# Performance work log

Measured on AMD Instinct MI355X. Metric: run time of the kernel, lower is better.

## Reference

```python
import jax, jax.numpy as jnp
import numpy as np

DEPTH = 6


def _interp_linear(x, out_len):
    # x: [B, C, Lin] -> [B, C, out_len], PyTorch mode='linear', align_corners=False
    lin = x.shape[-1]
    scale = lin / out_len
    coords = (jnp.arange(out_len, dtype=x.dtype) + 0.5) * scale - 0.5
    coords = jnp.clip(coords, 0.0, lin - 1)
    lo = jnp.floor(coords).astype(jnp.int32)
    hi = jnp.minimum(lo + 1, lin - 1)
    w = (coords - lo.astype(x.dtype))
    return x[..., lo] * (1.0 - w) + x[..., hi] * w


def _scale_features(x, conv_w, conv_b):
    # x: [B, C, L]; conv_w: [DEPTH, C, C, 3]; conv_b: [DEPTH, C]
    B, C, L = x.shape
    out = x
    for idx in range(DEPTH):
        k = 2 ** (idx + 1)
        pooled = out.reshape(B, C, L // k, k).mean(-1)  # avg_pool1d(kernel=k, stride=k)
        conv = jax.lax.conv_general_dilated(
            pooled, conv_w[idx], window_strides=(1,), padding=((1, 1),),
            dimension_numbers=("NCH", "OIH", "NCH"))
        conv = jax.nn.relu(conv + conv_b[idx][None, :, None])
        out = out + _interp_linear(conv, L)
    return out


def setup_inputs() -> dict:
    key = jax.random.key(0)
    ks = jax.random.split(key, 8)
    N, C = 8192, 512
    s = 1.0 / np.sqrt(C)
    return {
        "features": jax.random.normal(ks[0], (N, C), jnp.float32),
        "Wq": jax.random.normal(ks[1], (C, C), jnp.float32) * s,
        "Wk": jax.random.normal(ks[2], (C, C), jnp.float32) * s,
        "Wv": jax.random.normal(ks[3], (C, C), jnp.float32) * s,
        "Wo": jax.random.normal(ks[4], (C, C), jnp.float32) * s,
        "conv_w": jax.random.normal(ks[5], (DEPTH, C, C, 3), jnp.float32) * (1.0 / np.sqrt(3 * C)),
        "conv_b": jnp.zeros((DEPTH, C), jnp.float32),
        "num_subgraphs": 32,
        "subgraph_len": 256,
    }


def reference(features, Wq, Wk, Wv, Wo, conv_w, conv_b, num_subgraphs, subgraph_len):
    B, L = num_subgraphs, subgraph_len
    N, C = features.shape
    H = 8
    D = C // H
    x = features.reshape(B, L, C)

    # --- per-subgraph multi-head attention (pre_norm path, bn = identity) ---
    q = (x @ Wq).reshape(B, L, H, D)
    k = (x @ Wk).reshape(B, L, H, D)
    v = (x @ Wv).reshape(B, L, H, D)
    scores = jnp.einsum("blhd,bmhd->bhlm", q, k) / jnp.sqrt(jnp.array(D, x.dtype))
    attn = jax.nn.softmax(scores, axis=-1)
    ctx = jnp.einsum("bhlm,bmhd->blhd", attn, v).reshape(B, L, C)
    out = x + ctx @ Wo  # residual (dropout = identity at eval)

    # --- batched ScaleFeatures over subgraphs (ts.scatter.batched equivalent) ---
    local = _scale_features(out.transpose(0, 2, 1), conv_w, conv_b).transpose(0, 2, 1)
    out = out + local
    return out.reshape(N, C)
```

## Files before the change

### kernel.cpp

```cpp
#include <hip/hip_runtime.h>
#include <hip/hip_bf16.h>

typedef __bf16 bf16;
typedef __attribute__((ext_vector_type(8))) __bf16 bf16x8;
typedef __attribute__((ext_vector_type(4))) float f32x4;

#define GLDS16(gp, lp) __builtin_amdgcn_global_load_lds( \
    (const __attribute__((address_space(1))) void*)(gp),  \
    (__attribute__((address_space(3))) void*)(lp), 16, 0, 0)

template<int EPI, int BN>
__global__ __launch_bounds__(512)
void gemm_bt(const bf16* __restrict__ A, int lda, long sAb, long sAh,
             const bf16* __restrict__ Bt, int ldb, long sBb, long sBh,
             void* __restrict__ Cp, int ldc, long sCb, long sCh, long zC,
             int KC, int tilesN, float scale)
{
    constexpr int CT = BN / 64;
    constexpr int CW = 16 * CT;

    __shared__ __align__(16) bf16 Al[2][128 * 32];
    __shared__ __align__(16) bf16 Bl[2][BN * 32];
    __shared__ float red[1024];

    const int t    = threadIdx.x;
    const int lane = t & 63;
    const int w    = t >> 6;
    const int wr   = w >> 2, wc = w & 3;
    const int tm = blockIdx.x / tilesN, tn = blockIdx.x % tilesN;
    const int row0 = tm * 128, col0 = tn * BN;
    const int bb = blockIdx.y >> 3, bh = blockIdx.y & 7;
    const int koff = blockIdx.z * KC;

    const bf16* Ab = A  + (long)bb * sAb + (long)bh * sAh;
    const bf16* Bb = Bt + (long)bb * sBb + (long)bh * sBh;

    const int sr = t >> 2;
    const int sc = (t & 3) * 8;
    const long aoff  = (long)(row0 + sr) * lda + koff + sc;
    const long boff0 = (long)(col0 + sr) * ldb + koff + sc;
    const long boff1 = (long)(col0 + 128 + sr) * ldb + koff + sc;

    f32x4 acc[4][CT];
#pragma unroll
    for (int i = 0; i < 4; i++)
#pragma unroll
        for (int j = 0; j < CT; j++) acc[i][j] = (f32x4){0.f, 0.f, 0.f, 0.f};

    const int fr = lane & 15, hi = lane >> 4;
    const int nt = KC >> 5;
    int cur = 0;

    auto STAGE = [&](int buf, int kk) {
        GLDS16(Ab + aoff + kk, &Al[buf][w * 512]);
        if constexpr (BN >= 128) {
            GLDS16(Bb + boff0 + kk, &Bl[buf][w * 512]);
            if constexpr (BN == 256)
                GLDS16(Bb + boff1 + kk, &Bl[buf][4096 + w * 512]);
        } else {
            if (w < 4) GLDS16(Bb + boff0 + kk, &Bl[buf][w * 512]);
        }
    };

    STAGE(0, 0);
    __syncthreads();

    for (int tt = 0; tt < nt; ++tt) {
        if (tt + 1 < nt) STAGE(cur ^ 1, (tt + 1) * 32);
        bf16x8 af[4], bfr[CT];
#pragma unroll
        for (int rt = 0; rt < 4; rt++)
            af[rt] = *(const bf16x8*)&Al[cur][(wr * 64 + rt * 16 + fr) * 32 + hi * 8];
#pragma unroll
        for (int ct = 0; ct < CT; ct++)
            bfr[ct] = *(const bf16x8*)&Bl[cur][(wc * CW + ct * 16 + fr) * 32 + hi * 8];
#pragma unroll
        for (int rt = 0; rt < 4; rt++)
#pragma unroll
            for (int ct = 0; ct < CT; ct++)
                acc[rt][ct] = __builtin_amdgcn_mfma_f32_16x16x32_bf16(
                    af[rt], bfr[ct], acc[rt][ct], 0, 0, 0);
        __syncthreads();
        cur ^= 1;
    }

    const long cbase = (long)bb * sCb + (long)bh * sCh + (long)blockIdx.z * zC;

    if constexpr (EPI == 4) {
#pragma unroll
        for (int rt = 0; rt < 4; rt++)
#pragma unroll
            for (int ct = 0; ct < CT; ct++) acc[rt][ct] *= scale;

        float m[4][4];
#pragma unroll
        for (int rt = 0; rt < 4; rt++)
#pragma unroll
            for (int j = 0; j < 4; j++) {
                float mm = acc[rt][0][j];
#pragma unroll
                for (int ct = 1; ct < CT; ct++) mm = fmaxf(mm, acc[rt][ct][j]);
#pragma unroll
                for (int off = 1; off < 16; off <<= 1)
                    mm = fmaxf(mm, __shfl_xor(mm, off));
                m[rt][j] = mm;
            }
        if (fr == 0) {
#pragma unroll
            for (int rt = 0; rt < 4; rt++)
#pragma unroll
                for (int j = 0; j < 4; j++)
                    red[wc * 128 + wr * 64 + rt * 16 + hi * 4 + j] = m[rt][j];
        }
        __syncthreads();
#pragma unroll
        for (int rt = 0; rt < 4; rt++)
#pragma unroll
            for (int j = 0; j < 4; j++) {
                const int rl = wr * 64 + rt * 16 + hi * 4 + j;
                m[rt][j] = fmaxf(fmaxf(red[rl], red[128 + rl]),
                                 fmaxf(red[256 + rl], red[384 + rl]));
            }
        float ss[4][4];
#pragma unroll
        for (int rt = 0; rt < 4; rt++)
#pragma unroll
            for (int j = 0; j < 4; j++) ss[rt][j] = 0.f;
#pragma unroll
        for (int rt = 0; rt < 4; rt++)
#pragma unroll
            for (int ct = 0; ct < CT; ct++)
#pragma unroll
                for (int j = 0; j < 4; j++) {
                    const float e = __expf(acc[rt][ct][j] - m[rt][j]);
                    acc[rt][ct][j] = e;
                    ss[rt][j] += e;
                }
#pragma unroll
        for (int rt = 0; rt < 4; rt++)
#pragma unroll
            for (int j = 0; j < 4; j++) {
#pragma unroll
                for (int off = 1; off < 16; off <<= 1)
                    ss[rt][j] += __shfl_xor(ss[rt][j], off);
            }
        if (fr == 0) {
#pragma unroll
            for (int rt = 0; rt < 4; rt++)
#pragma unroll
                for (int j = 0; j < 4; j++)
                    red[512 + wc * 128 + wr * 64 + rt * 16 + hi * 4 + j] = ss[rt][j];
        }
        __syncthreads();
#pragma unroll
        for (int rt = 0; rt < 4; rt++)
#pragma unroll
            for (int j = 0; j < 4; j++) {
                const int rl = wr * 64 + rt * 16 + hi * 4 + j;
                m[rt][j] = 1.f / (red[512 + rl] + red[640 + rl] +
                                  red[768 + rl] + red[896 + rl]);
            }
        bf16* P = (bf16*)Cp;
#pragma unroll
        for (int rt = 0; rt < 4; rt++)
#pragma unroll
            for (int j = 0; j < 4; j++) {
                const int row = row0 + wr * 64 + rt * 16 + hi * 4 + j;
#pragma unroll
                for (int ct = 0; ct < CT; ct++) {
                    const int col = col0 + wc * CW + ct * 16 + fr;
                    P[cbase + (long)row * ldc + col] = (bf16)(acc[rt][ct][j] * m[rt][j]);
                }
            }
        return;
    }

#pragma unroll
    for (int rt = 0; rt < 4; rt++) {
#pragma unroll
        for (int j = 0; j < 4; j++) {
            const int row = row0 + wr * 64 + rt * 16 + hi * 4 + j;
#pragma unroll
            for (int ct = 0; ct < CT; ct++) {
                const int col = col0 + wc * CW + ct * 16 + fr;
                const float v = acc[rt][ct][j];
                const long idx = cbase + (long)row * ldc + col;
                if constexpr (EPI == 0) {
                    ((bf16*)Cp)[idx] = (bf16)v;
                } else {
                    ((float*)Cp)[idx] = v * scale;
                }
            }
        }
    }
}

__global__ void reduce_partials(const float* __restrict__ part,
                                float* __restrict__ outb,
                                long stride4, int P, int n4)
{
    const int i = blockIdx.x * 256 + threadIdx.x;
    if (i >= n4) return;
    float4 s = ((const float4*)part)[i];
    for (int p = 1; p < P; p++) {
        const float4 v = ((const float4*)part)[(long)p * stride4 + i];
        s.x += v.x; s.y += v.y; s.z += v.z; s.w += v.w;
    }
    ((float4*)outb)[i] = s;
}

__global__ void cvt_f32_bf16(const float* __restrict__ in, bf16* __restrict__ out, int n4)
{
    const int i = blockIdx.x * 256 + threadIdx.x;
    if (i < n4) {
        const float4 v = *(const float4*)&in[(long)i * 4];
        union { bf16 h[4]; ushort4 u; } o;
        o.h[0] = (bf16)v.x; o.h[1] = (bf16)v.y; o.h[2] = (bf16)v.z; o.h[3] = (bf16)v.w;
        *(ushort4*)&out[(long)i * 4] = o.u;
    }
}

__global__ __launch_bounds__(256)
void wtrans(const float* __restrict__ Wq, const float* __restrict__ Wk,
            const float* __restrict__ Wv, const float* __restrict__ Wo,
            bf16* __restrict__ wqkv_t, bf16* __restrict__ wo_t)
{
    __shared__ __align__(16) float T[64][68];
    const int z = blockIdx.z;
    const float* src = (z == 0) ? Wq : (z == 1) ? Wk : (z == 2) ? Wv : Wo;
    bf16* dst = (z < 3) ? (wqkv_t + (long)z * 262144) : wo_t;
    const int r0 = blockIdx.x * 64, c0 = blockIdx.y * 64;
    const int t  = threadIdx.x;
    const int rl = t >> 2;
    const int cq = (t & 3) * 16;
#pragma unroll
    for (int i = 0; i < 4; i++) {
        const float4 v = *(const float4*)&src[(long)(r0 + rl) * 512 + c0 + cq + i * 4];
        T[cq + i * 4 + 0][rl] = v.x;
        T[cq + i * 4 + 1][rl] = v.y;
        T[cq + i * 4 + 2][rl] = v.z;
        T[cq + i * 4 + 3][rl] = v.w;
    }
    __syncthreads();
#pragma unroll
    for (int i = 0; i < 4; i++) {
        const float4 v = *(const float4*)&T[rl][cq + i * 4];
        union { bf16 h[4]; ushort4 u; } o;
        o.h[0] = (bf16)v.x; o.h[1] = (bf16)v.y; o.h[2] = (bf16)v.z; o.h[3] = (bf16)v.w;
        *(ushort4*)&dst[(long)(c0 + rl) * 512 + r0 + cq + i * 4] = o.u;
    }
}

__global__ __launch_bounds__(256)
void vtrans(const bf16* __restrict__ qkv, bf16* __restrict__ vt)
{
    __shared__ __align__(16) bf16 T[64][72];
    const int t  = threadIdx.x;
    const int l0 = blockIdx.x * 64, j0 = blockIdx.y * 64, b = blockIdx.z;
    const int r  = t >> 3;
    const int c8 = (t & 7) * 8;
#pragma unroll
    for (int p = 0; p < 2; p++) {
        const int rr = r + p * 32;
        bf16 v[8];
        *(uint4*)v = *(const uint4*)&qkv[(long)(b * 256 + l0 + rr) * 1536 + 1024 + j0 + c8];
#pragma unroll
        for (int i = 0; i < 8; i++) T[c8 + i][rr] = v[i];
    }
    __syncthreads();
#pragma unroll
    for (int p = 0; p < 2; p++) {
        const int rr = r + p * 32;
        const uint4 val = *(const uint4*)&T[rr][c8];
        *(uint4*)&vt[(long)(b * 512 + j0 + rr) * 256 + l0 + c8] = val;
    }
}

__device__ inline void ic_scatter(bf16* __restrict__ icb, int lp, int Ld, float pooled)
{
    const bf16 pb = (bf16)pooled;
    icb[(long)lp * 1536 + 1] = pb;
    if (lp + 1 < Ld) icb[(long)(lp + 1) * 1536] = pb;
    if (lp > 0)      icb[(long)(lp - 1) * 1536 + 2] = pb;
    if (lp == 0)      icb[0] = (bf16)0.f;
    if (lp == Ld - 1) icb[(long)(Ld - 1) * 1536 + 2] = (bf16)0.f;
}

__global__ void cascade_first(const float* __restrict__ features,
                              const float* __restrict__ p0,
                              const float* __restrict__ p1,
                              float* __restrict__ out,
                              float* __restrict__ sf,
                              bf16* __restrict__ ic)
{
    const int idx = blockIdx.x * 256 + threadIdx.x;
    const int c  = idx & 511;
    const int lp = (idx >> 9) & 127;
    const int b  = idx >> 16;
    const long e0 = (long)(b * 256 + lp * 2) * 512 + c;
    const long e1 = e0 + 512;
    const float a0 = features[e0] + p0[e0] + p1[e0];
    const float a1 = features[e1] + p0[e1] + p1[e1];
    out[e0] = a0; out[e1] = a1;
    sf[e0]  = a0; sf[e1]  = a1;
    ic_scatter(ic + (long)b * 128 * 1536 + (long)c * 3, lp, 128, (a0 + a1) * 0.5f);
}

__global__ void cascade_mid(const float* __restrict__ conv,
                            const float* __restrict__ bias_p,
                            float* __restrict__ sf,
                            bf16* __restrict__ ic,
                            int ldshift, int k, float invk, float scale)
{
    const int idx = blockIdx.x * 256 + threadIdx.x;
    const int Ld = 1 << ldshift;
    const int c  = idx & 511;
    const int lp = (idx >> 9) & (Ld - 1);
    const int b  = idx >> (9 + ldshift);
    const int Lprev = Ld << 1;
    const float bias = bias_p[c];
    float* sfp = sf + ((long)b * 256 + (long)lp * k) * 512 + c;
    const float* cvb = conv + (long)b * Lprev * 512 + c;
    float s = 0.f;
    for (int i = 0; i < k; i++) {
        const int j = lp * k + i;
        float coords = (j + 0.5f) * scale - 0.5f;
        coords = fminf(fmaxf(coords, 0.f), (float)(Lprev - 1));
        const int lo = (int)coords;
        const int hi2 = min(lo + 1, Lprev - 1);
        const float w = coords - (float)lo;
        const float vlo = fmaxf(cvb[(long)lo * 512] + bias, 0.f);
        const float vhi = fmaxf(cvb[(long)hi2 * 512] + bias, 0.f);
        const float v = sfp[(long)i * 512] + vlo * (1.f - w) + vhi * w;
        sfp[(long)i * 512] = v;
        s += v;
    }
    ic_scatter(ic + (long)b * Ld * 1536 + (long)c * 3, lp, Ld, s * invk);
}

__global__ void upsample_final(const float* __restrict__ conv,
                               const float* __restrict__ bias_p,
                               const float* __restrict__ sf,
                               float* __restrict__ outp)
{
    const int idx = blockIdx.x * 256 + threadIdx.x;
    const int c = idx & 511;
    const int j = (idx >> 9) & 255;
    const int b = idx >> 17;
    const float bias = bias_p[c];
    float coords = (j + 0.5f) * (4.f / 256.f) - 0.5f;
    coords = fminf(fmaxf(coords, 0.f), 3.f);
    const int lo = (int)coords;
    const int hi2 = min(lo + 1, 3);
    const float w = coords - (float)lo;
    const long rb = (long)b * 4 * 512 + c;
    const float vlo = fmaxf(conv[rb + (long)lo * 512] + bias, 0.f);
    const float vhi = fmaxf(conv[rb + (long)hi2 * 512] + bias, 0.f);
    outp[idx] = outp[idx] + sf[idx] + vlo * (1.f - w) + vhi * w;
}

static const long OFF_XB    = 0;
static const long OFF_WQKV  = 8388608;
static const long OFF_WO    = 9961472;
static const long OFF_WCONV = 10485760;
static const long OFF_QKV   = 19922944;
static const long OFF_VT    = 45088768;
static const long OFF_P     = 53477376;
static const long OFF_CTX   = 87031808;
static const long OFF_WPART = 95420416;
static const long OFF_IC    = 128974848;
static const long OFF_CONVA = 141557760;
static const long OFF_CONVB = 149946368;
static const long OFF_SF    = 154140672;

extern "C" void kernel_launch(void* const* d_in, const int* in_sizes, int n_in,
                              void* d_out, int out_size, void* d_ws, size_t ws_size,
                              hipStream_t stream)
{
    const float* features = (const float*)d_in[0];
    const float* Wq = (const float*)d_in[1];
    const float* Wk = (const float*)d_in[2];
    const float* Wv = (const float*)d_in[3];
    const float* Wo = (const float*)d_in[4];
    const float* conv_w = (const float*)d_in[5];
    const float* conv_b = (const float*)d_in[6];
    float* out = (float*)d_out;

    char* ws = (char*)d_ws;
    bf16* xb     = (bf16*)(ws + OFF_XB);
    bf16* wqkv_t = (bf16*)(ws + OFF_WQKV);
    bf16* wo_t   = (bf16*)(ws + OFF_WO);
    bf16* wconv  = (bf16*)(ws + OFF_WCONV);
    bf16* qkv    = (bf16*)(ws + OFF_QKV);
    bf16* vt     = (bf16*)(ws + OFF_VT);
    bf16* P      = (bf16*)(ws + OFF_P);
    bf16* ctx    = (bf16*)(ws + OFF_CTX);
    float* wpart = (float*)(ws + OFF_WPART);
    bf16* ic     = (bf16*)(ws + OFF_IC);
    float* convA = (float*)(ws + OFF_CONVA);
    float* convB = (float*)(ws + OFF_CONVB);
    float* sf    = (float*)(ws + OFF_SF);
    float* convbuf[2] = {convA, convB};

    cvt_f32_bf16<<<4096, 256, 0, stream>>>(features, xb, 1048576);
    cvt_f32_bf16<<<4608, 256, 0, stream>>>(conv_w, wconv, 1179648);
    wtrans<<<dim3(8, 8, 4), 256, 0, stream>>>(Wq, Wk, Wv, Wo, wqkv_t, wo_t);

    gemm_bt<0, 128><<<dim3(768, 1, 1), 512, 0, stream>>>(
        xb, 512, 0, 0, wqkv_t, 512, 0, 0, qkv, 1536, 0, 0, 0,
        512, 12, 1.f);

    vtrans<<<dim3(4, 8, 32), 256, 0, stream>>>(qkv, vt);

    gemm_bt<4, 256><<<dim3(2, 256, 1), 512, 0, stream>>>(
        qkv, 1536, 393216, 64,
        qkv + 512, 1536, 393216, 64,
        P, 256, 524288, 65536, 0,
        64, 1, 0.125f);

    gemm_bt<0, 64><<<dim3(2, 256, 1), 512, 0, stream>>>(
        P, 256, 524288, 65536,
        vt, 256, 131072, 16384,
        ctx, 512, 131072, 64, 0,
        256, 1, 1.f);

    gemm_bt<1, 128><<<dim3(256, 1, 2), 512, 0, stream>>>(
        ctx, 512, 0, 0, wo_t, 512, 0, 0,
        wpart, 512, 0, 0, 4194304,
        256, 4, 1.f);

    static const int SPL[6] = {4, 8, 16, 16, 16, 16};

    cascade_first<<<8192, 256, 0, stream>>>(
        features, wpart, wpart + 4194304, out, sf, ic);
    {
        const int M = 4096;
        gemm_bt<1, 128><<<dim3(128, 1, SPL[0]), 512, 0, stream>>>(
            ic, 1536, 0, 0, wconv, 1536, 0, 0,
            wpart, 512, 0, 0, (long)M * 512,
            1536 / SPL[0], 4, 1.f);
        reduce_partials<<<(M * 128) / 256, 256, 0, stream>>>(
            wpart, convbuf[0], (long)M * 128, SPL[0], M * 128);
    }

    for (int d = 1; d < 6; d++) {
        const int ldshift = 7 - d;
        const int Ld = 1 << ldshift;
        const int k  = 2 << d;
        const int M  = 32 * Ld;
        cascade_mid<<<64 * Ld, 256, 0, stream>>>(
            convbuf[(d - 1) & 1], conv_b + (d - 1) * 512, sf, ic,
            ldshift, k, 1.0f / (float)k, (float)(2 * Ld) / 256.f);
        gemm_bt<1, 128><<<dim3((M / 128) * 4, 1, SPL[d]), 512, 0, stream>>>(
            ic, 1536, 0, 0,
            wconv + (long)d * 786432, 1536, 0, 0,
            wpart, 512, 0, 0, (long)M * 512,
            1536 / SPL[d], 4, 1.f);
        reduce_partials<<<(M * 128) / 256, 256, 0, stream>>>(
            wpart, convbuf[d & 1], (long)M * 128, SPL[d], M * 128);
    }

    upsample_final<<<16384, 256, 0, stream>>>(
        convbuf[1], conv_b + 5 * 512, sf, out);
}
```

Measured before the change: 368.4 us.

## Fuse QK^T, softmax and PV into a single attention kernel

```diff
diff --git a/kernel.cpp b/kernel.cpp
--- a/kernel.cpp
+++ b/kernel.cpp
@@ -21,7 +21,6 @@
 
     __shared__ __align__(16) bf16 Al[2][128 * 32];
     __shared__ __align__(16) bf16 Bl[2][BN * 32];
-    __shared__ float red[1024];
 
     const int t    = threadIdx.x;
     const int lane = t & 63;
@@ -85,95 +84,6 @@
     }
 
     const long cbase = (long)bb * sCb + (long)bh * sCh + (long)blockIdx.z * zC;
-
-    if constexpr (EPI == 4) {
-#pragma unroll
-        for (int rt = 0; rt < 4; rt++)
-#pragma unroll
-            for (int ct = 0; ct < CT; ct++) acc[rt][ct] *= scale;
-
-        float m[4][4];
-#pragma unroll
-        for (int rt = 0; rt < 4; rt++)
-#pragma unroll
-            for (int j = 0; j < 4; j++) {
-                float mm = acc[rt][0][j];
-#pragma unroll
-                for (int ct = 1; ct < CT; ct++) mm = fmaxf(mm, acc[rt][ct][j]);
-#pragma unroll
-                for (int off = 1; off < 16; off <<= 1)
-                    mm = fmaxf(mm, __shfl_xor(mm, off));
-                m[rt][j] = mm;
-            }
-        if (fr == 0) {
-#pragma unroll
-            for (int rt = 0; rt < 4; rt++)
-#pragma unroll
-                for (int j = 0; j < 4; j++)
-                    red[wc * 128 + wr * 64 + rt * 16 + hi * 4 + j] = m[rt][j];
-        }
-        __syncthreads();
-#pragma unroll
-        for (int rt = 0; rt < 4; rt++)
-#pragma unroll
-            for (int j = 0; j < 4; j++) {
-                const int rl = wr * 64 + rt * 16 + hi * 4 + j;
-                m[rt][j] = fmaxf(fmaxf(red[rl], red[128 + rl]),
-                                 fmaxf(red[256 + rl], red[384 + rl]));
-            }
-        float ss[4][4];
-#pragma unroll
-        for (int rt = 0; rt < 4; rt++)
-#pragma unroll
-            for (int j = 0; j < 4; j++) ss[rt][j] = 0.f;
-#pragma unroll
-        for (int rt = 0; rt < 4; rt++)
-#pragma unroll
-            for (int ct = 0; ct < CT; ct++)
-#pragma unroll
-                for (int j = 0; j < 4; j++) {
-                    const float e = __expf(acc[rt][ct][j] - m[rt][j]);
-                    acc[rt][ct][j] = e;
-                    ss[rt][j] += e;
-                }
-#pragma unroll
-        for (int rt = 0; rt < 4; rt++)
-#pragma unroll
-            for (int j = 0; j < 4; j++) {
-#pragma unroll
-                for (int off = 1; off < 16; off <<= 1)
-                    ss[rt][j] += __shfl_xor(ss[rt][j], off);
-            }
-        if (fr == 0) {
-#pragma unroll
-            for (int rt = 0; rt < 4; rt++)
-#pragma unroll
-                for (int j = 0; j < 4; j++)
-                    red[512 + wc * 128 + wr * 64 + rt * 16 + hi * 4 + j] = ss[rt][j];
-        }
-        __syncthreads();
-#pragma unroll
-        for (int rt = 0; rt < 4; rt++)
-#pragma unroll
-            for (int j = 0; j < 4; j++) {
-                const int rl = wr * 64 + rt * 16 + hi * 4 + j;
-                m[rt][j] = 1.f / (red[512 + rl] + red[640 + rl] +
-                                  red[768 + rl] + red[896 + rl]);
-            }
-        bf16* P = (bf16*)Cp;
-#pragma unroll
-        for (int rt = 0; rt < 4; rt++)
-#pragma unroll
-            for (int j = 0; j < 4; j++) {
-                const int row = row0 + wr * 64 + rt * 16 + hi * 4 + j;
-#pragma unroll
-                for (int ct = 0; ct < CT; ct++) {
-                    const int col = col0 + wc * CW + ct * 16 + fr;
-                    P[cbase + (long)row * ldc + col] = (bf16)(acc[rt][ct][j] * m[rt][j]);
-                }
-            }
-        return;
-    }
 
 #pragma unroll
     for (int rt = 0; rt < 4; rt++) {
@@ -195,6 +105,187 @@
     }
 }
 
+__global__ __launch_bounds__(512)
+void attn_fused(const bf16* __restrict__ qkv, bf16* __restrict__ ctx)
+{
+    __shared__ __align__(16) char smem[105472];
+    bf16*  Pl  = (bf16*)smem;
+    bf16*  Vt  = (bf16*)(smem + 67584);
+    float* red = (float*)(smem + 101376);
+
+    const int t    = threadIdx.x;
+    const int lane = t & 63;
+    const int w    = t >> 6;
+    const int wr   = w >> 2, wc = w & 3;
+    const int fr = lane & 15, hi = lane >> 4;
+    const int row0 = blockIdx.x * 128;
+    const int b = blockIdx.y >> 3, h = blockIdx.y & 7;
+
+    const bf16* qbase = qkv + (long)b * 393216 + h * 64;
+    const bf16* kbase = qbase + 512;
+    const bf16* vbase = qbase + 1024;
+
+    bf16x8 vreg[4];
+#pragma unroll
+    for (int p = 0; p < 4; p++) {
+        const int q = p * 512 + t;
+        const int m  = q >> 3;
+        const int c8 = (q & 7) * 8;
+        vreg[p] = *(const bf16x8*)(vbase + (long)m * 1536 + c8);
+    }
+
+    f32x4 acc[4][4];
+#pragma unroll
+    for (int i = 0; i < 4; i++)
+#pragma unroll
+        for (int j = 0; j < 4; j++) acc[i][j] = (f32x4){0.f, 0.f, 0.f, 0.f};
+
+#pragma unroll
+    for (int kc = 0; kc < 2; kc++) {
+        bf16x8 af[4], bfr[4];
+#pragma unroll
+        for (int rt = 0; rt < 4; rt++) {
+            const int l = row0 + wr * 64 + rt * 16 + fr;
+            af[rt] = *(const bf16x8*)(qbase + (long)l * 1536 + kc * 32 + hi * 8);
+        }
+#pragma unroll
+        for (int ct = 0; ct < 4; ct++) {
+            const int m = wc * 64 + ct * 16 + fr;
+            bfr[ct] = *(const bf16x8*)(kbase + (long)m * 1536 + kc * 32 + hi * 8);
+        }
+#pragma unroll
+        for (int rt = 0; rt < 4; rt++)
+#pragma unroll
+            for (int ct = 0; ct < 4; ct++)
+                acc[rt][ct] = __builtin_amdgcn_mfma_f32_16x16x32_bf16(
+                    af[rt], bfr[ct], acc[rt][ct], 0, 0, 0);
+    }
+
+#pragma unroll
+    for (int p = 0; p < 4; p++) {
+        const int q = p * 512 + t;
+        const int m  = q >> 3;
+        const int c8 = (q & 7) * 8;
+#pragma unroll
+        for (int i = 0; i < 8; i++)
+            Vt[(c8 + i) * 264 + m] = vreg[p][i];
+    }
+
+#pragma unroll
+    for (int rt = 0; rt < 4; rt++)
+#pragma unroll
+        for (int ct = 0; ct < 4; ct++) acc[rt][ct] *= 0.125f;
+
+    float m4[4][4];
+#pragma unroll
+    for (int rt = 0; rt < 4; rt++)
+#pragma unroll
+        for (int j = 0; j < 4; j++) {
+            float mm = acc[rt][0][j];
+#pragma unroll
+            for (int ct = 1; ct < 4; ct++) mm = fmaxf(mm, acc[rt][ct][j]);
+#pragma unroll
+            for (int off = 1; off < 16; off <<= 1)
+                mm = fmaxf(mm, __shfl_xor(mm, off));
+            m4[rt][j] = mm;
+        }
+    if (fr == 0) {
+#pragma unroll
+        for (int rt = 0; rt < 4; rt++)
+#pragma unroll
+            for (int j = 0; j < 4; j++)
+                red[wc * 128 + wr * 64 + rt * 16 + hi * 4 + j] = m4[rt][j];
+    }
+    __syncthreads();
+#pragma unroll
+    for (int rt = 0; rt < 4; rt++)
+#pragma unroll
+        for (int j = 0; j < 4; j++) {
+            const int rl = wr * 64 + rt * 16 + hi * 4 + j;
+            m4[rt][j] = fmaxf(fmaxf(red[rl], red[128 + rl]),
+                              fmaxf(red[256 + rl], red[384 + rl]));
+        }
+    float ss[4][4];
+#pragma unroll
+    for (int rt = 0; rt < 4; rt++)
+#pragma unroll
+        for (int j = 0; j < 4; j++) ss[rt][j] = 0.f;
+#pragma unroll
+    for (int rt = 0; rt < 4; rt++)
+#pragma unroll
+        for (int ct = 0; ct < 4; ct++)
+#pragma unroll
+            for (int j = 0; j < 4; j++) {
+                const float e = __expf(acc[rt][ct][j] - m4[rt][j]);
+                acc[rt][ct][j] = e;
+                ss[rt][j] += e;
+            }
+#pragma unroll
+    for (int rt = 0; rt < 4; rt++)
+#pragma unroll
+        for (int j = 0; j < 4; j++) {
+#pragma unroll
+            for (int off = 1; off < 16; off <<= 1)
+                ss[rt][j] += __shfl_xor(ss[rt][j], off);
+        }
+    if (fr == 0) {
+#pragma unroll
+        for (int rt = 0; rt < 4; rt++)
+#pragma unroll
+            for (int j = 0; j < 4; j++)
+                red[512 + wc * 128 + wr * 64 + rt * 16 + hi * 4 + j] = ss[rt][j];
+    }
+    __syncthreads();
+#pragma unroll
+    for (int rt = 0; rt < 4; rt++)
+#pragma unroll
+        for (int j = 0; j < 4; j++) {
+            const int rl = wr * 64 + rt * 16 + hi * 4 + j;
+            m4[rt][j] = 1.f / (red[512 + rl] + red[640 + rl] +
+                               red[768 + rl] + red[896 + rl]);
+        }
+
+#pragma unroll
+    for (int rt = 0; rt < 4; rt++)
+#pragma unroll
+        for (int j = 0; j < 4; j++) {
+            const int rl = wr * 64 + rt * 16 + hi * 4 + j;
+#pragma unroll
+            for (int ct = 0; ct < 4; ct++) {
+                const int col = wc * 64 + ct * 16 + fr;
+                Pl[rl * 264 + col] = (bf16)(acc[rt][ct][j] * m4[rt][j]);
+            }
+        }
+    __syncthreads();
+
+    f32x4 acc2[4];
+#pragma unroll
+    for (int i = 0; i < 4; i++) acc2[i] = (f32x4){0.f, 0.f, 0.f, 0.f};
+
+#pragma unroll
+    for (int ks = 0; ks < 8; ks++) {
+        const int k0 = ks * 32;
+        bf16x8 af2[4], bfr2;
+#pragma unroll
+        for (int rt = 0; rt < 4; rt++)
+            af2[rt] = *(const bf16x8*)&Pl[(wr * 64 + rt * 16 + fr) * 264 + k0 + hi * 8];
+        bfr2 = *(const bf16x8*)&Vt[(wc * 16 + fr) * 264 + k0 + hi * 8];
+#pragma unroll
+        for (int rt = 0; rt < 4; rt++)
+            acc2[rt] = __builtin_amdgcn_mfma_f32_16x16x32_bf16(
+                af2[rt], bfr2, acc2[rt], 0, 0, 0);
+    }
+
+#pragma unroll
+    for (int rt = 0; rt < 4; rt++)
+#pragma unroll
+        for (int j = 0; j < 4; j++) {
+            const int l = row0 + wr * 64 + rt * 16 + hi * 4 + j;
+            const int d = wc * 16 + fr;
+            ctx[(long)(b * 256 + l) * 512 + h * 64 + d] = (bf16)(acc2[rt][j]);
+        }
+}
+
 __global__ void reduce_partials(const float* __restrict__ part,
                                 float* __restrict__ outb,
                                 long stride4, int P, int n4)
@@ -248,31 +339,6 @@
         union { bf16 h[4]; ushort4 u; } o;
         o.h[0] = (bf16)v.x; o.h[1] = (bf16)v.y; o.h[2] = (bf16)v.z; o.h[3] = (bf16)v.w;
         *(ushort4*)&dst[(long)(c0 + rl) * 512 + r0 + cq + i * 4] = o.u;
-    }
-}
-
-__global__ __launch_bounds__(256)
-void vtrans(const bf16* __restrict__ qkv, bf16* __restrict__ vt)
-{
-    __shared__ __align__(16) bf16 T[64][72];
-    const int t  = threadIdx.x;
-    const int l0 = blockIdx.x * 64, j0 = blockIdx.y * 64, b = blockIdx.z;
-    const int r  = t >> 3;
-    const int c8 = (t & 7) * 8;
-#pragma unroll
-    for (int p = 0; p < 2; p++) {
-        const int rr = r + p * 32;
-        bf16 v[8];
-        *(uint4*)v = *(const uint4*)&qkv[(long)(b * 256 + l0 + rr) * 1536 + 1024 + j0 + c8];
-#pragma unroll
-        for (int i = 0; i < 8; i++) T[c8 + i][rr] = v[i];
-    }
-    __syncthreads();
-#pragma unroll
-    for (int p = 0; p < 2; p++) {
-        const int rr = r + p * 32;
-        const uint4 val = *(const uint4*)&T[rr][c8];
-        *(uint4*)&vt[(long)(b * 512 + j0 + rr) * 256 + l0 + c8] = val;
     }
 }
 
@@ -364,8 +430,6 @@
 static const long OFF_WO    = 9961472;
 static const long OFF_WCONV = 10485760;
 static const long OFF_QKV   = 19922944;
-static const long OFF_VT    = 45088768;
-static const long OFF_P     = 53477376;
 static const long OFF_CTX   = 87031808;
 static const long OFF_WPART = 95420416;
 static const long OFF_IC    = 128974848;
@@ -392,8 +456,6 @@
     bf16* wo_t   = (bf16*)(ws + OFF_WO);
     bf16* wconv  = (bf16*)(ws + OFF_WCONV);
     bf16* qkv    = (bf16*)(ws + OFF_QKV);
-    bf16* vt     = (bf16*)(ws + OFF_VT);
-    bf16* P      = (bf16*)(ws + OFF_P);
     bf16* ctx    = (bf16*)(ws + OFF_CTX);
     float* wpart = (float*)(ws + OFF_WPART);
     bf16* ic     = (bf16*)(ws + OFF_IC);
@@ -410,19 +472,7 @@
         xb, 512, 0, 0, wqkv_t, 512, 0, 0, qkv, 1536, 0, 0, 0,
         512, 12, 1.f);
 
-    vtrans<<<dim3(4, 8, 32), 256, 0, stream>>>(qkv, vt);
-
-    gemm_bt<4, 256><<<dim3(2, 256, 1), 512, 0, stream>>>(
-        qkv, 1536, 393216, 64,
-        qkv + 512, 1536, 393216, 64,
-        P, 256, 524288, 65536, 0,
-        64, 1, 0.125f);
-
-    gemm_bt<0, 64><<<dim3(2, 256, 1), 512, 0, stream>>>(
-        P, 256, 524288, 65536,
-        vt, 256, 131072, 16384,
-        ctx, 512, 131072, 64, 0,
-        256, 1, 1.f);
+    attn_fused<<<dim3(2, 256), 512, 0, stream>>>(qkv, ctx);
 
     gemm_bt<1, 128><<<dim3(256, 1, 2), 512, 0, stream>>>(
         ctx, 512, 0, 0, wo_t, 512, 0, 0,
```

New measurement: 361.5 us. Within noise of the previous version (-1.9%).
